# Performance work log

Measured on AMD Instinct MI355X. Metric: run time of the kernel, lower is better.

Reference implementation:

```python
import math
import jax, jax.numpy as jnp
import numpy as np

NUM_CODES = 8192
CODE_DIM = 256
COMMITMENT = 0.25
DECAY = 0.99
EPS = 1e-5


def setup_inputs() -> dict:
    key = jax.random.key(0)
    k1, k2 = jax.random.split(key)
    z = jax.random.normal(k1, (16, CODE_DIM, 32, 32), dtype=jnp.float32)
    # codebook init ~ U(-sqrt(3/K), sqrt(3/K)) as in EmbeddingEMA
    lim = math.sqrt(3.0 / NUM_CODES)
    weight = jax.random.uniform(k2, (NUM_CODES, CODE_DIM), dtype=jnp.float32,
                                minval=-lim, maxval=lim)
    cluster_size = jnp.zeros((NUM_CODES,), dtype=jnp.float32)
    embed_avg = weight.copy()
    return {"z": z, "weight": weight, "cluster_size": cluster_size,
            "embed_avg": embed_avg}


def reference(z, weight, cluster_size, embed_avg):
    B, C, H, W = z.shape
    z_bhwc = jnp.transpose(z, (0, 2, 3, 1))            # [B,H,W,C]
    z_flat = z_bhwc.reshape(-1, C)                     # [N,C], N = B*H*W
    N = z_flat.shape[0]

    # Pairwise squared distances: |z|^2 + |w|^2 - 2 z.w  -> [N, K]
    dist = (jnp.sum(z_flat ** 2, axis=1, keepdims=True)
            + jnp.sum(weight ** 2, axis=1)
            - 2.0 * jnp.einsum('nd,kd->nk', z_flat, weight))
    idx = jnp.argmin(dist, axis=1)                     # [N] int

    z_q = weight[idx].reshape(z_bhwc.shape)            # gather, [B,H,W,C]

    # usage stats via segment reductions (avoids dense one-hot [N,K])
    counts = jax.ops.segment_sum(jnp.ones((N,), z.dtype), idx,
                                 num_segments=NUM_CODES)        # [K]
    avg_use = counts / N
    perplexity = jnp.exp(-jnp.sum(avg_use * jnp.log(avg_use + 1e-10)))

    # EMA updates (training mode); z_q for this pass uses the OLD weight
    embed_sum = jax.ops.segment_sum(z_flat, idx, num_segments=NUM_CODES)  # [K,C]
    new_cluster_size = DECAY * cluster_size + (1.0 - DECAY) * counts
    new_embed_avg = DECAY * embed_avg + (1.0 - DECAY) * embed_sum
    n = jnp.sum(new_cluster_size)
    smoothed = (new_cluster_size + EPS) / (n + NUM_CODES * EPS) * n
    new_weight = new_embed_avg / smoothed[:, None]

    # commitment loss (z_q detached) and straight-through estimator
    loss = COMMITMENT * jnp.mean((jax.lax.stop_gradient(z_q) - z_bhwc) ** 2)
    z_q_ste = z_bhwc + jax.lax.stop_gradient(z_q - z_bhwc)
    z_q_out = jnp.transpose(z_q_ste, (0, 3, 1, 2))     # [B,C,H,W]
    idx_out = idx.reshape(B, H, W)

    return (z_q_out, loss, idx_out, perplexity,
            new_weight, new_cluster_size, new_embed_avg)
```

## Files before the change

kernel.cpp:

```cpp
#include <hip/hip_runtime.h>

typedef _Float16 f16;
typedef _Float16 f16x8 __attribute__((ext_vector_type(8)));
typedef float f32x4 __attribute__((ext_vector_type(4)));

#define K_CODES 8192
#define C_DIM   256
#define N_TOTAL 16384
#define HWSZ    1024

#define O_ZQ   0
#define O_LOSS 4194304
#define O_IDX  4194305
#define O_PERP 4210689
#define O_W    4210690
#define O_CS   6307842
#define O_EA   6316034

#define WS_WN    0
#define WS_IDX   8192
#define WS_CNTI  24576
#define WS_CNTF  32768
#define WS_SEG   40960
#define WS_CUR   49152
#define WS_PERM  57344
#define WS_LPART 73728
#define WS_NTOT  77824
#define WS_CAND  81920

#define NQ 8
#define QCODES (K_CODES / NQ)
#define NTILES (QCODES / 32)
#define NCAND  (2 * NQ)

__global__ __launch_bounds__(256) void k_prep(const float* __restrict__ z,
                                              const float* __restrict__ w,
                                              f16* __restrict__ zhi,
                                              f16* __restrict__ zlo,
                                              f16* __restrict__ whi,
                                              float* __restrict__ wn,
                                              int* __restrict__ cnt_i)
{
    const int bid = blockIdx.x;
    const int tid = threadIdx.x;
    if (bid < 512) {
        __shared__ float zs[32 * C_DIM];
        const int m0  = bid * 32;
        const int b   = m0 >> 10;
        const int hw0 = m0 & 1023;
        {
            const int i4  = (tid & 7) << 2;
            const int c0s = tid >> 3;
            const float* zp = z + (size_t)b * (C_DIM * HWSZ) + hw0 + i4;
            for (int c = c0s; c < C_DIM; c += 32) {
                float4 v = *(const float4*)(zp + (size_t)c * HWSZ);
                float vv[4] = {v.x, v.y, v.z, v.w};
#pragma unroll
                for (int j = 0; j < 4; ++j) {
                    int r = i4 + j;
                    zs[r * C_DIM + (c ^ (((r >> 1) & 3) << 2))] = vv[j];
                }
            }
        }
        __syncthreads();
        const int r   = tid >> 3;
        const int cc0 = (tid & 7) * 32;
        const int rsw = ((r >> 1) & 3) << 2;
        const size_t obase = (size_t)(m0 + r) * C_DIM + cc0;
#pragma unroll
        for (int p = 0; p < 4; ++p) {
            f16x8 h, l;
#pragma unroll
            for (int e = 0; e < 8; ++e) {
                float v = -2.f * zs[r * C_DIM + ((cc0 + p * 8 + e) ^ rsw)];
                f16 hh = (f16)v;
                h[e] = hh;
                l[e] = (f16)(v - (float)hh);
            }
            *(f16x8*)(zhi + obase + p * 8) = h;
            *(f16x8*)(zlo + obase + p * 8) = l;
        }
    } else {
        const int pb = bid - 512;
        if (pb < 8) {
            const int t0 = pb * 1024 + tid * 4;
            *(int4*)&cnt_i[t0] = (int4){0, 0, 0, 0};
        }
        const size_t i8 = ((size_t)pb * 256 + tid) * 8;
        float4 a = *(const float4*)(w + i8);
        float4 b = *(const float4*)(w + i8 + 4);
        float vv[8] = {a.x, a.y, a.z, a.w, b.x, b.y, b.z, b.w};
        f16x8 h;
        float s = 0.f;
#pragma unroll
        for (int e = 0; e < 8; ++e) {
            h[e] = (f16)vv[e];
            s += vv[e] * vv[e];
        }
        *(f16x8*)(whi + i8) = h;
#pragma unroll
        for (int d = 1; d < 32; d <<= 1) s += __shfl_xor(s, d, 64);
        if ((tid & 31) == 0) wn[i8 >> 8] = s;
    }
}

__global__ __launch_bounds__(512, 4) void k_select(
    const f16* __restrict__ zhi,
    const f16* __restrict__ whi,
    const float* __restrict__ wn, int* __restrict__ cand)
{
    __shared__ f16 wls[2][32 * C_DIM];

    const int tid  = threadIdx.x;
    const int wave = tid >> 6;
    const int lane = tid & 63;
    const int l15  = lane & 15;
    const int l4   = lane >> 4;

    const int rowbase = blockIdx.x * 256 + wave * 32;
    const int q       = blockIdx.y;
    const int code0   = q * QCODES;

    f16x8 ah[2][8];
#pragma unroll
    for (int mf = 0; mf < 2; ++mf) {
        const f16* zbh = zhi + (size_t)(rowbase + mf * 16 + l15) * C_DIM + l4 * 8;
#pragma unroll
        for (int ks = 0; ks < 8; ++ks)
            ah[mf][ks] = *(const f16x8*)(zbh + ks * 32);
    }

    const int s_code = tid >> 4;
    const int s_ch   = tid & 15;
    const int kk0    = s_ch * 8;
    const int kk1    = kk0 + 128;
    const int ssw    = (s_code & 7) << 3;
    const int s_lds0 = s_code * C_DIM + (kk0 ^ ssw);
    const int s_lds1 = s_code * C_DIM + (kk1 ^ ssw);

    const int bsw  = (l15 & 7) << 3;
    const int b_k0 = l4 * 8;

    float p1[8], p2[8];
#pragma unroll
    for (int s = 0; s < 8; ++s) { p1[s] = 3.4e38f; p2[s] = 3.4e38f; }

    {
        const f16* g = whi + (size_t)(code0 + s_code) * C_DIM;
        f16x8 a0 = *(const f16x8*)(g + kk0);
        f16x8 a1 = *(const f16x8*)(g + kk1);
        *(f16x8*)&wls[0][s_lds0] = a0;
        *(f16x8*)&wls[0][s_lds1] = a1;
    }

    for (int t = 0; t < NTILES; ++t) {
        __syncthreads();
        const int buf = t & 1;
        const bool more = (t + 1) < NTILES;
        f16x8 nr0, nr1;
        if (more) {
            const f16* g = whi + (size_t)(code0 + (t + 1) * 32 + s_code) * C_DIM;
            nr0 = *(const f16x8*)(g + kk0);
            nr1 = *(const f16x8*)(g + kk1);
        }

        const int tbase = t * 32;
        const float wnv0 = wn[code0 + tbase + l15];
        const float wnv1 = wn[code0 + tbase + 16 + l15];
        f32x4 acc[2][2];
#pragma unroll
        for (int mf = 0; mf < 2; ++mf) {
            acc[mf][0] = (f32x4){wnv0, wnv0, wnv0, wnv0};
            acc[mf][1] = (f32x4){wnv1, wnv1, wnv1, wnv1};
        }

#pragma unroll
        for (int ks = 0; ks < 8; ++ks) {
#pragma unroll
            for (int nf = 0; nf < 2; ++nf) {
                const int e = (nf * 16 + l15) * C_DIM + ((ks * 32 + b_k0) ^ bsw);
                f16x8 bh = *(const f16x8*)&wls[buf][e];
#pragma unroll
                for (int mf = 0; mf < 2; ++mf)
                    acc[mf][nf] = __builtin_amdgcn_mfma_f32_16x16x32_f16(ah[mf][ks], bh, acc[mf][nf], 0, 0, 0);
            }
        }

#pragma unroll
        for (int nf = 0; nf < 2; ++nf) {
            const int cl = tbase + nf * 16 + l15;
#pragma unroll
            for (int mf = 0; mf < 2; ++mf)
#pragma unroll
                for (int r = 0; r < 4; ++r) {
                    const float u = __uint_as_float(
                        (__float_as_uint(acc[mf][nf][r]) & 0xFFFFF800u) | (unsigned)cl);
                    const int s = mf * 4 + r;
                    p2[s] = fminf(p2[s], fmaxf(p1[s], u));
                    p1[s] = fminf(p1[s], u);
                }
        }

        if (more) {
            *(f16x8*)&wls[buf ^ 1][s_lds0] = nr0;
            *(f16x8*)&wls[buf ^ 1][s_lds1] = nr1;
        }
    }

#pragma unroll
    for (int s = 0; s < 8; ++s) {
        float a1 = p1[s], a2 = p2[s];
#pragma unroll
        for (int st = 1; st <= 8; st <<= 1) {
            float b1 = __shfl_xor(a1, st, 64);
            float b2 = __shfl_xor(a2, st, 64);
            a2 = fminf(fminf(a2, b2), fmaxf(a1, b1));
            a1 = fminf(a1, b1);
        }
        if (l15 == 0) {
            const int row = rowbase + (s >> 2) * 16 + l4 * 4 + (s & 3);
            cand[row * NCAND + q * 2 + 0] = code0 + (int)(__float_as_uint(a1) & 0x7FFu);
            cand[row * NCAND + q * 2 + 1] = code0 + (int)(__float_as_uint(a2) & 0x7FFu);
        }
    }
}

__global__ __launch_bounds__(256) void k_rerank(const float* __restrict__ z,
                                                const float* __restrict__ w,
                                                const int* __restrict__ cand,
                                                int* __restrict__ idx,
                                                float* __restrict__ oidx,
                                                int* __restrict__ cnt_i)
{
#pragma clang fp contract(off)
    __shared__ float zs[32 * C_DIM];
    const int tid = threadIdx.x;
    const int m0  = blockIdx.x * 32;
    const int b   = m0 >> 10;
    const int hw0 = m0 & 1023;
    {
        const int i4  = (tid & 7) << 2;
        const int c0s = tid >> 3;
        const float* zp = z + (size_t)b * (C_DIM * HWSZ) + hw0 + i4;
        for (int c = c0s; c < C_DIM; c += 32) {
            float4 v = *(const float4*)(zp + (size_t)c * HWSZ);
            float vv[4] = {v.x, v.y, v.z, v.w};
#pragma unroll
            for (int j = 0; j < 4; ++j) {
                int r = i4 + j;
                zs[r * C_DIM + (c ^ (((r >> 1) & 3) << 2))] = vv[j];
            }
        }
    }
    __syncthreads();

    const int tx  = tid & 15;
    const int ty  = tid >> 4;
    const int zsw = (ty & 3) << 2;

#pragma unroll
    for (int j = 0; j < 2; ++j) {
        const int r   = ty * 2 + j;
        const int row = m0 + r;

        float blk[2];
#pragma unroll
        for (int bb = 0; bb < 2; ++bb) {
            float tarr[8];
#pragma unroll
            for (int t8 = 0; t8 < 8; ++t8) {
                float zz = zs[r * C_DIM + ((bb * 128 + t8 * 16 + tx) ^ zsw)];
                tarr[t8] = zz * zz;
            }
            float p01 = tarr[0] + tarr[1];
            float p23 = tarr[2] + tarr[3];
            float p45 = tarr[4] + tarr[5];
            float p67 = tarr[6] + tarr[7];
            float W = (p01 + p23) + (p45 + p67);
            W += __shfl_xor(W, 8, 64);
            W += __shfl_xor(W, 4, 64);
            W += __shfl_xor(W, 2, 64);
            W += __shfl_xor(W, 1, 64);
            blk[bb] = W;
        }
        const float af = blk[0] + blk[1];

        float bestd = 3.4e38f; int besti = 0x7fffffff;
        for (int c = 0; c < NCAND; ++c) {
            const int ci = cand[row * NCAND + c];
            const float* wp = w + (size_t)ci * C_DIM;
            double ss = 0, qq = 0;
            const int cb = tx * 16;
#pragma unroll
            for (int cc = 0; cc < 16; cc += 4) {
                const int col = cb + cc;
                float4 zv = *(const float4*)&zs[r * C_DIM + (col ^ zsw)];
                float4 wa = *(const float4*)(wp + col);
                ss += (double)zv.x * wa.x + (double)zv.y * wa.y + (double)zv.z * wa.z + (double)zv.w * wa.w;
                qq += (double)wa.x * wa.x + (double)wa.y * wa.y + (double)wa.z * wa.z + (double)wa.w * wa.w;
            }
#pragma unroll
            for (int st = 1; st <= 8; st <<= 1) {
                ss += __shfl_xor(ss, st, 64);
                qq += __shfl_xor(qq, st, 64);
            }
            const float d = (af + (float)qq) - (float)(2.0 * ss);
            if (d < bestd || (d == bestd && ci < besti)) { bestd = d; besti = ci; }
        }
        if (tx == 0) {
            idx[row]  = besti;
            oidx[row] = (float)besti;
            atomicAdd(&cnt_i[besti], 1);
        }
    }
}

__global__ __launch_bounds__(256) void k_scanstats(const int* __restrict__ cnt_i,
                                                   const float* __restrict__ cs,
                                                   int* __restrict__ seg,
                                                   int* __restrict__ cur,
                                                   float* __restrict__ cnt_f,
                                                   float* __restrict__ ntot,
                                                   float* __restrict__ out_perp)
{
    __shared__ int ls[256];
    const int tid = threadIdx.x;
    const int base = tid * 32;
    int loc[32];
    int s = 0;
#pragma unroll
    for (int i = 0; i < 32; ++i) { loc[i] = s; s += cnt_i[base + i]; }
    ls[tid] = s;
    __syncthreads();
    for (int off = 1; off < 256; off <<= 1) {
        int v = (tid >= off) ? ls[tid - off] : 0;
        __syncthreads();
        ls[tid] += v;
        __syncthreads();
    }
    const int excl = (tid == 0) ? 0 : ls[tid - 1];
    float sn = 0.f, se = 0.f;
#pragma unroll
    for (int i = 0; i < 32; ++i) {
        const int k = base + i;
        const int cn = cnt_i[k];
        const int o = excl + loc[i];
        seg[k] = o;
        cur[k] = o;
        cnt_f[k] = (float)cn;
        sn += 0.99f * cs[k] + 0.01f * (float)cn;
        float p = (float)cn * (1.f / (float)N_TOTAL);
        se += p * logf(p + 1e-10f);
    }
#pragma unroll
    for (int d = 1; d < 64; d <<= 1) {
        sn += __shfl_xor(sn, d, 64);
        se += __shfl_xor(se, d, 64);
    }
    __shared__ float r[8];
    if ((tid & 63) == 0) { int wv = tid >> 6; r[wv] = sn; r[4 + wv] = se; }
    __syncthreads();
    if (tid == 0) {
        *ntot = r[0] + r[1] + r[2] + r[3];
        *out_perp = expf(-(r[4] + r[5] + r[6] + r[7]));
    }
}

__global__ __launch_bounds__(256) void k_scatter(const int* __restrict__ idx,
                                                 int* __restrict__ cur,
                                                 int* __restrict__ perm)
{
    const int n = blockIdx.x * 256 + threadIdx.x;
    const int p = atomicAdd(&cur[idx[n]], 1);
    perm[p] = n;
}

__global__ __launch_bounds__(256) void k_esum(const f16* __restrict__ zhi,
                                              const f16* __restrict__ zlo,
                                              const int* __restrict__ seg,
                                              const int* __restrict__ cnt_i,
                                              const int* __restrict__ perm,
                                              float* __restrict__ esum)
{
    const int k  = blockIdx.x;
    const int c  = threadIdx.x;
    const int s0 = seg[k];
    const int cn = cnt_i[k];
    float acc = 0.f;
    for (int i = 0; i < cn; ++i) {
        const int n = perm[s0 + i];
        acc += (float)zhi[(size_t)n * C_DIM + c] + (float)zlo[(size_t)n * C_DIM + c];
    }
    esum[(size_t)k * C_DIM + c] = -0.5f * acc;
}

__global__ __launch_bounds__(256) void k_zq(const float* __restrict__ z,
                                            const float* __restrict__ w,
                                            const int* __restrict__ idx,
                                            float* __restrict__ zq,
                                            float* __restrict__ lpart)
{
    const int bid = blockIdx.x;
    const int b   = bid >> 8;
    const int c   = bid & 255;
    const int tid = threadIdx.x;
    const int hw4 = tid * 4;
    const size_t zoff = (size_t)b * (C_DIM * HWSZ) + (size_t)c * HWSZ + hw4;

    float4 zv = *(const float4*)(z + zoff);
    const int nb = b * HWSZ + hw4;
    int4 iv = *(const int4*)(idx + nb);

    float4 wq;
    wq.x = w[(size_t)iv.x * C_DIM + c];
    wq.y = w[(size_t)iv.y * C_DIM + c];
    wq.z = w[(size_t)iv.z * C_DIM + c];
    wq.w = w[(size_t)iv.w * C_DIM + c];
    *(float4*)(zq + zoff) = wq;

    float dx = wq.x - zv.x, dy = wq.y - zv.y, dz = wq.z - zv.z, dw = wq.w - zv.w;
    float ls = dx * dx + dy * dy + dz * dz + dw * dw;

#pragma unroll
    for (int d = 1; d < 64; d <<= 1) ls += __shfl_xor(ls, d, 64);
    __shared__ float red[4];
    if ((tid & 63) == 0) red[tid >> 6] = ls;
    __syncthreads();
    if (tid == 0) lpart[bid] = red[0] + red[1] + red[2] + red[3];
}

__global__ __launch_bounds__(256) void k_update(const float* __restrict__ cs,
                                                const float* __restrict__ cnt,
                                                const float* __restrict__ ea,
                                                const float* __restrict__ esum,
                                                const float* __restrict__ ntot,
                                                const float* __restrict__ lpart,
                                                float* __restrict__ o_w,
                                                float* __restrict__ o_cs,
                                                float* __restrict__ o_ea,
                                                float* __restrict__ out_loss)
{
    const int k = blockIdx.x;
    const int c = threadIdx.x;
    if (k == K_CODES) {
        float sl = 0.f;
        for (int i = c; i < 4096; i += 256) sl += lpart[i];
#pragma unroll
        for (int d = 1; d < 64; d <<= 1) sl += __shfl_xor(sl, d, 64);
        __shared__ float r[4];
        if ((c & 63) == 0) r[c >> 6] = sl;
        __syncthreads();
        if (c == 0)
            *out_loss = 0.25f * (r[0] + r[1] + r[2] + r[3]) * (1.f / 4194304.f);
        return;
    }
    float ncs = 0.99f * cs[k] + 0.01f * cnt[k];
    float n = *ntot;
    float sm = (ncs + 1e-5f) / (n + (float)K_CODES * 1e-5f) * n;
    if (c == 0) o_cs[k] = ncs;
    size_t o = (size_t)k * C_DIM + c;
    float v = 0.99f * ea[o] + 0.01f * esum[o];
    o_ea[o] = v;
    o_w[o]  = v / sm;
}

extern "C" void kernel_launch(void* const* d_in, const int* in_sizes, int n_in,
                              void* d_out, int out_size, void* d_ws, size_t ws_size,
                              hipStream_t stream)
{
    const float* z  = (const float*)d_in[0];
    const float* w  = (const float*)d_in[1];
    const float* cs = (const float*)d_in[2];
    const float* ea = (const float*)d_in[3];
    float* out = (float*)d_out;
    float* ws  = (float*)d_ws;

    float* wn    = ws + WS_WN;
    int*   idx   = (int*)(ws + WS_IDX);
    int*   cnt_i = (int*)(ws + WS_CNTI);
    float* cnt_f = ws + WS_CNTF;
    int*   seg   = (int*)(ws + WS_SEG);
    int*   cur   = (int*)(ws + WS_CUR);
    int*   perm  = (int*)(ws + WS_PERM);
    float* lpart = ws + WS_LPART;
    float* ntot  = ws + WS_NTOT;
    int*   cand  = (int*)(ws + WS_CAND);
    float* esum  = out + O_EA;

    f16* zhi = (f16*)(out + O_ZQ);
    f16* zlo = zhi + (size_t)N_TOTAL * C_DIM;
    f16* whi = (f16*)(out + O_W + 2);

    k_prep     <<<1536, 256, 0, stream>>>(z, w, zhi, zlo, whi, wn, cnt_i);
    k_select   <<<dim3(N_TOTAL / 256, NQ), 512, 0, stream>>>(zhi, whi, wn, cand);
    k_rerank   <<<N_TOTAL / 32, 256, 0, stream>>>(z, w, cand, idx, out + O_IDX, cnt_i);
    k_scanstats<<<1, 256, 0, stream>>>(cnt_i, cs, seg, cur, cnt_f, ntot, out + O_PERP);
    k_scatter  <<<N_TOTAL / 256, 256, 0, stream>>>(idx, cur, perm);
    k_esum     <<<K_CODES, 256, 0, stream>>>(zhi, zlo, seg, cnt_i, perm, esum);
    k_zq       <<<16 * 256, 256, 0, stream>>>(z, w, idx, out + O_ZQ, lpart);
    k_update   <<<K_CODES + 1, 256, 0, stream>>>(cs, cnt_f, ea, esum, ntot, lpart,
                                                 out + O_W, out + O_CS, out + O_EA,
                                                 out + O_LOSS);
}
```

Before: 187.3 us.

## Fuse scatter into scan kernel and fuse embed-sum with EMA update

The per-sample scatter into code-sorted order now runs inside the single-block scan kernel, using shared-memory cursors instead of a global cursor array. The embed-sum reduction is fused directly into the EMA weight/avg update, so the intermediate sum is no longer written to and re-read from global memory. The loss reduction moves into its own tiny kernel. This removes a launch and an 8 MB round trip, but it serialises the scatter onto a single block.

```diff
diff --git a/kernel.cpp b/kernel.cpp
--- a/kernel.cpp
+++ b/kernel.cpp
@@ -20,9 +20,7 @@
 #define WS_WN    0
 #define WS_IDX   8192
 #define WS_CNTI  24576
-#define WS_CNTF  32768
 #define WS_SEG   40960
-#define WS_CUR   49152
 #define WS_PERM  57344
 #define WS_LPART 73728
 #define WS_NTOT  77824
@@ -317,13 +315,14 @@
 
 __global__ __launch_bounds__(256) void k_scanstats(const int* __restrict__ cnt_i,
                                                    const float* __restrict__ cs,
+                                                   const int* __restrict__ idx,
                                                    int* __restrict__ seg,
-                                                   int* __restrict__ cur,
-                                                   float* __restrict__ cnt_f,
+                                                   int* __restrict__ perm,
                                                    float* __restrict__ ntot,
                                                    float* __restrict__ out_perp)
 {
     __shared__ int ls[256];
+    __shared__ int cur_l[K_CODES];
     const int tid = threadIdx.x;
     const int base = tid * 32;
     int loc[32];
@@ -346,12 +345,16 @@
         const int cn = cnt_i[k];
         const int o = excl + loc[i];
         seg[k] = o;
-        cur[k] = o;
-        cnt_f[k] = (float)cn;
+        cur_l[k] = o;
         sn += 0.99f * cs[k] + 0.01f * (float)cn;
         float p = (float)cn * (1.f / (float)N_TOTAL);
         se += p * logf(p + 1e-10f);
     }
+    __syncthreads();
+    for (int n = tid; n < N_TOTAL; n += 256) {
+        const int p = atomicAdd(&cur_l[idx[n]], 1);
+        perm[p] = n;
+    }
 #pragma unroll
     for (int d = 1; d < 64; d <<= 1) {
         sn += __shfl_xor(sn, d, 64);
@@ -366,21 +369,17 @@
     }
 }
 
-__global__ __launch_bounds__(256) void k_scatter(const int* __restrict__ idx,
-                                                 int* __restrict__ cur,
-                                                 int* __restrict__ perm)
-{
-    const int n = blockIdx.x * 256 + threadIdx.x;
-    const int p = atomicAdd(&cur[idx[n]], 1);
-    perm[p] = n;
-}
-
-__global__ __launch_bounds__(256) void k_esum(const f16* __restrict__ zhi,
-                                              const f16* __restrict__ zlo,
-                                              const int* __restrict__ seg,
-                                              const int* __restrict__ cnt_i,
-                                              const int* __restrict__ perm,
-                                              float* __restrict__ esum)
+__global__ __launch_bounds__(256) void k_update(const f16* __restrict__ zhi,
+                                                const f16* __restrict__ zlo,
+                                                const int* __restrict__ seg,
+                                                const int* __restrict__ cnt_i,
+                                                const int* __restrict__ perm,
+                                                const float* __restrict__ cs,
+                                                const float* __restrict__ ea,
+                                                const float* __restrict__ ntot,
+                                                float* __restrict__ o_w,
+                                                float* __restrict__ o_cs,
+                                                float* __restrict__ o_ea)
 {
     const int k  = blockIdx.x;
     const int c  = threadIdx.x;
@@ -391,7 +390,15 @@
         const int n = perm[s0 + i];
         acc += (float)zhi[(size_t)n * C_DIM + c] + (float)zlo[(size_t)n * C_DIM + c];
     }
-    esum[(size_t)k * C_DIM + c] = -0.5f * acc;
+    const float es = -0.5f * acc;
+    const float ncs = 0.99f * cs[k] + 0.01f * (float)cn;
+    const float n = *ntot;
+    const float sm = (ncs + 1e-5f) / (n + (float)K_CODES * 1e-5f) * n;
+    if (c == 0) o_cs[k] = ncs;
+    const size_t o = (size_t)k * C_DIM + c;
+    const float v = 0.99f * ea[o] + 0.01f * es;
+    o_ea[o] = v;
+    o_w[o]  = v / sm;
 }
 
 __global__ __launch_bounds__(256) void k_zq(const float* __restrict__ z,
@@ -429,39 +436,19 @@
     if (tid == 0) lpart[bid] = red[0] + red[1] + red[2] + red[3];
 }
 
-__global__ __launch_bounds__(256) void k_update(const float* __restrict__ cs,
-                                                const float* __restrict__ cnt,
-                                                const float* __restrict__ ea,
-                                                const float* __restrict__ esum,
-                                                const float* __restrict__ ntot,
-                                                const float* __restrict__ lpart,
-                                                float* __restrict__ o_w,
-                                                float* __restrict__ o_cs,
-                                                float* __restrict__ o_ea,
-                                                float* __restrict__ out_loss)
-{
-    const int k = blockIdx.x;
-    const int c = threadIdx.x;
-    if (k == K_CODES) {
-        float sl = 0.f;
-        for (int i = c; i < 4096; i += 256) sl += lpart[i];
-#pragma unroll
-        for (int d = 1; d < 64; d <<= 1) sl += __shfl_xor(sl, d, 64);
-        __shared__ float r[4];
-        if ((c & 63) == 0) r[c >> 6] = sl;
-        __syncthreads();
-        if (c == 0)
-            *out_loss = 0.25f * (r[0] + r[1] + r[2] + r[3]) * (1.f / 4194304.f);
-        return;
-    }
-    float ncs = 0.99f * cs[k] + 0.01f * cnt[k];
-    float n = *ntot;
-    float sm = (ncs + 1e-5f) / (n + (float)K_CODES * 1e-5f) * n;
-    if (c == 0) o_cs[k] = ncs;
-    size_t o = (size_t)k * C_DIM + c;
-    float v = 0.99f * ea[o] + 0.01f * esum[o];
-    o_ea[o] = v;
-    o_w[o]  = v / sm;
+__global__ __launch_bounds__(256) void k_loss(const float* __restrict__ lpart,
+                                              float* __restrict__ out_loss)
+{
+    const int tid = threadIdx.x;
+    float sl = 0.f;
+    for (int i = tid; i < 4096; i += 256) sl += lpart[i];
+#pragma unroll
+    for (int d = 1; d < 64; d <<= 1) sl += __shfl_xor(sl, d, 64);
+    __shared__ float r[4];
+    if ((tid & 63) == 0) r[tid >> 6] = sl;
+    __syncthreads();
+    if (tid == 0)
+        *out_loss = 0.25f * (r[0] + r[1] + r[2] + r[3]) * (1.f / 4194304.f);
 }
 
 extern "C" void kernel_launch(void* const* d_in, const int* in_sizes, int n_in,
@@ -478,14 +465,11 @@
     float* wn    = ws + WS_WN;
     int*   idx   = (int*)(ws + WS_IDX);
     int*   cnt_i = (int*)(ws + WS_CNTI);
-    float* cnt_f = ws + WS_CNTF;
     int*   seg   = (int*)(ws + WS_SEG);
-    int*   cur   = (int*)(ws + WS_CUR);
     int*   perm  = (int*)(ws + WS_PERM);
     float* lpart = ws + WS_LPART;
     float* ntot  = ws + WS_NTOT;
     int*   cand  = (int*)(ws + WS_CAND);
-    float* esum  = out + O_EA;
 
     f16* zhi = (f16*)(out + O_ZQ);
     f16* zlo = zhi + (size_t)N_TOTAL * C_DIM;
@@ -494,11 +478,9 @@
     k_prep     <<<1536, 256, 0, stream>>>(z, w, zhi, zlo, whi, wn, cnt_i);
     k_select   <<<dim3(N_TOTAL / 256, NQ), 512, 0, stream>>>(zhi, whi, wn, cand);
     k_rerank   <<<N_TOTAL / 32, 256, 0, stream>>>(z, w, cand, idx, out + O_IDX, cnt_i);
-    k_scanstats<<<1, 256, 0, stream>>>(cnt_i, cs, seg, cur, cnt_f, ntot, out + O_PERP);
-    k_scatter  <<<N_TOTAL / 256, 256, 0, stream>>>(idx, cur, perm);
-    k_esum     <<<K_CODES, 256, 0, stream>>>(zhi, zlo, seg, cnt_i, perm, esum);
+    k_scanstats<<<1, 256, 0, stream>>>(cnt_i, cs, idx, seg, perm, ntot, out + O_PERP);
+    k_update   <<<K_CODES, 256, 0, stream>>>(zhi, zlo, seg, cnt_i, perm, cs, ea, ntot,
+                                             out + O_W, out + O_CS, out + O_EA);
     k_zq       <<<16 * 256, 256, 0, stream>>>(z, w, idx, out + O_ZQ, lpart);
-    k_update   <<<K_CODES + 1, 256, 0, stream>>>(cs, cnt_f, ea, esum, ntot, lpart,
-                                                 out + O_W, out + O_CS, out + O_EA,
-                                                 out + O_LOSS);
-}
+    k_loss     <<<1, 256, 0, stream>>>(lpart, out + O_LOSS);
+}
```

Measured after the change: 202.6 us. 1.08x slower.
